# Kernel optimization log

Measured on AMD Instinct MI355X. Metric: run time of the kernel, lower is better.

Reference implementation:

```python
import jax, jax.numpy as jnp
import numpy as np


def setup_inputs() -> dict:
    key = jax.random.key(0)
    x = jax.random.normal(key, (8192, 4096), dtype=jnp.float32)
    return {"x": x, "k": 1}


def reference(x, k):
    # torch.linalg.svdvals returns singular values in descending order;
    # jnp.linalg.svd with compute_uv=False does the same.
    s = jnp.linalg.svd(x, compute_uv=False)  # [min(m, n)], descending
    return jnp.sum(s[:k] ** 2)
```

## Files before the change

kernel.cpp:

```cpp
#include <hip/hip_runtime.h>
#include <hip/hip_fp16.h>
#include <math.h>


#define NROWS 8192
#define NCOLS 4096
#define T_STEPS 16
#define NBLK 512
#define RPB 16
#define SPIN_LIMIT 200000L

typedef float f32x4_t __attribute__((ext_vector_type(4)));

__device__ __forceinline__ unsigned ic_ld_u32(const unsigned* p) {
    unsigned v;
    asm volatile("global_load_dword %0, %1, off sc0 sc1\n\ts_waitcnt vmcnt(0)"
                 : "=v"(v) : "v"(p) : "memory");
    return v;
}
__device__ __forceinline__ float ic_ld_f32(const float* p) {
    float v;
    asm volatile("global_load_dword %0, %1, off sc0 sc1\n\ts_waitcnt vmcnt(0)"
                 : "=v"(v) : "v"(p) : "memory");
    return v;
}
__device__ __forceinline__ void ic_st_u32(unsigned* p, unsigned v) {
    asm volatile("global_store_dword %0, %1, off sc0 sc1"
                 :: "v"(p), "v"(v) : "memory");
}
__device__ __forceinline__ void ic_st_f32(float* p, float v) {
    asm volatile("global_store_dword %0, %1, off sc0 sc1"
                 :: "v"(p), "v"(v) : "memory");
}
__device__ __forceinline__ void ic_st4_f32(float* p, float4 v) {
    f32x4_t x; x.x = v.x; x.y = v.y; x.z = v.z; x.w = v.w;
    asm volatile("global_store_dwordx4 %0, %1, off sc0 sc1"
                 :: "v"(p), "v"(x) : "memory");
}
__device__ __forceinline__ unsigned ic_sum4_u32(const unsigned* p0, const unsigned* p1,
                                                const unsigned* p2, const unsigned* p3) {
    unsigned a, b, c, d;
    asm volatile(
        "global_load_dword %0, %4, off sc0 sc1\n\t"
        "global_load_dword %1, %5, off sc0 sc1\n\t"
        "global_load_dword %2, %6, off sc0 sc1\n\t"
        "global_load_dword %3, %7, off sc0 sc1\n\t"
        "s_waitcnt vmcnt(0)"
        : "=&v"(a), "=&v"(b), "=&v"(c), "=&v"(d)
        : "v"(p0), "v"(p1), "v"(p2), "v"(p3) : "memory");
    return a + b + c + d;
}
__device__ __forceinline__ void ic_ld4_f32x4(const float* p0, const float* p1,
                                             const float* p2, const float* p3,
                                             float4& ao, float4& bo, float4& co, float4& do_) {
    f32x4_t a, b, c, d;
    asm volatile(
        "global_load_dwordx4 %0, %4, off sc0 sc1\n\t"
        "global_load_dwordx4 %1, %5, off sc0 sc1\n\t"
        "global_load_dwordx4 %2, %6, off sc0 sc1\n\t"
        "global_load_dwordx4 %3, %7, off sc0 sc1\n\t"
        "s_waitcnt vmcnt(0)"
        : "=&v"(a), "=&v"(b), "=&v"(c), "=&v"(d)
        : "v"(p0), "v"(p1), "v"(p2), "v"(p3) : "memory");
    ao = make_float4(a.x, a.y, a.z, a.w);
    bo = make_float4(b.x, b.y, b.z, b.w);
    co = make_float4(c.x, c.y, c.z, c.w);
    do_ = make_float4(d.x, d.y, d.z, d.w);
}

__device__ __forceinline__ void up8(const float4& p, float* f) {
    const __half2* h = (const __half2*)&p;
    float2 t0 = __half22float2(h[0]);
    float2 t1 = __half22float2(h[1]);
    float2 t2 = __half22float2(h[2]);
    float2 t3 = __half22float2(h[3]);
    f[0] = t0.x; f[1] = t0.y; f[2] = t1.x; f[3] = t1.y;
    f[4] = t2.x; f[5] = t2.y; f[6] = t3.x; f[7] = t3.y;
}
__device__ __forceinline__ float4 pack8(const float4& a, const float4& b) {
    union { float4 f4; __half2 h2[4]; } u;
    u.h2[0] = __halves2half2(__float2half_rn(a.x), __float2half_rn(a.y));
    u.h2[1] = __halves2half2(__float2half_rn(a.z), __float2half_rn(a.w));
    u.h2[2] = __halves2half2(__float2half_rn(b.x), __float2half_rn(b.y));
    u.h2[3] = __halves2half2(__float2half_rn(b.z), __float2half_rn(b.w));
    return u.f4;
}

__device__ __forceinline__ void gbar(unsigned* arrive, unsigned* release,
                                     unsigned* errw, unsigned gen, int bid) {
    __syncthreads();
    if (threadIdx.x == 0) {
        asm volatile("s_waitcnt vmcnt(0)" ::: "memory");
        __hip_atomic_fetch_add(&arrive[(bid & 7) * 16], 1u,
                               __ATOMIC_RELAXED, __HIP_MEMORY_SCOPE_AGENT);
        if (ic_ld_u32(errw) == 0) {
            long iters = 0;
            if (bid == 0) {
                const unsigned target = gen * NBLK;
                for (;;) {
                    unsigned s = ic_sum4_u32(&arrive[0], &arrive[16], &arrive[32], &arrive[48])
                               + ic_sum4_u32(&arrive[64], &arrive[80], &arrive[96], &arrive[112]);
                    if (s >= target) break;
                    if (++iters > SPIN_LIMIT) { ic_st_u32(errw, gen); break; }
                    if ((iters & 255) == 0 && ic_ld_u32(errw)) break;
                    __builtin_amdgcn_s_sleep(2);
                }
                ic_st_u32(release, gen);
            } else {
                while (ic_ld_u32(release) < gen) {
                    if (++iters > SPIN_LIMIT) { ic_st_u32(errw, gen); break; }
                    if ((iters & 255) == 0 && ic_ld_u32(errw)) break;
                    __builtin_amdgcn_s_sleep(2);
                }
            }
        }
    }
    __syncthreads();
}

__global__ __launch_bounds__(256, 2) void lanczos_fused(const float* __restrict__ A,
                                                        float* __restrict__ ws,
                                                        float* __restrict__ out) {
    __shared__ __align__(16) float smem[192];
    float* slots = ws + 12288;
    unsigned* arrive = (unsigned*)(ws + 12416);
    unsigned* release = (unsigned*)(ws + 12416) + 192;
    unsigned* errw = (unsigned*)(ws + 12416) + 200;
    float* partials = ws + 262144;
    const int tid = threadIdx.x;
    const int bid = blockIdx.x;
    const int gtid = bid * 256 + tid;
    const int cA = tid * 8, cB = 2048 + tid * 8;
    unsigned gen = 0;

    float4 arA[RPB], arB[RPB];
    {
        const float* base = A + (size_t)bid * RPB * NCOLS;
#pragma unroll
        for (int r = 0; r < RPB; ++r) {
            const float* rowp = base + (size_t)r * NCOLS;
            float4 a0 = *(const float4*)(rowp + cA);
            float4 a1 = *(const float4*)(rowp + cA + 4);
            float4 b0 = *(const float4*)(rowp + cB);
            float4 b1 = *(const float4*)(rowp + cB + 4);
            arA[r] = pack8(a0, a1);
            arB[r] = pack8(b0, b1);
        }
        if (gtid < NCOLS) {
            unsigned h = (unsigned)gtid * 2654435761u;
            h ^= h >> 16; h *= 2246822519u; h ^= h >> 13;
            ic_st_f32(ws + 4096 + gtid, (h & 1u) ? 0.015625f : -0.015625f);
            ic_st_f32(ws + gtid, 0.f);
            if (gtid < 128)
                ic_st_f32(slots + gtid, (gtid == 64 || gtid == 65) ? 1.f : 0.f);
        }
    }
    gbar(arrive, release, errw, ++gen, bid);

    for (int j = 1; j <= T_STEPS; ++j) {
        const float* rc = ws + 4096 * (j % 3);
        const float* rp = ws + 4096 * ((j + 2) % 3);
        float* wt = ws + 4096 * ((j + 1) % 3);

        {
            int lane = tid & 63;
            float inv = rsqrtf(fmaxf(ic_ld_f32(&slots[64 + j]), 1e-30f));
            float vA[8], vB[8];
            {
                float4 x, y, z, w4;
                ic_ld4_f32x4(rc + cA, rc + cA + 4, rc + cB, rc + cB + 4, x, y, z, w4);
                vA[0] = x.x * inv; vA[1] = x.y * inv; vA[2] = x.z * inv; vA[3] = x.w * inv;
                vA[4] = y.x * inv; vA[5] = y.y * inv; vA[6] = y.z * inv; vA[7] = y.w * inv;
                vB[0] = z.x * inv; vB[1] = z.y * inv; vB[2] = z.z * inv; vB[3] = z.w * inv;
                vB[4] = w4.x * inv; vB[5] = w4.y * inv; vB[6] = w4.z * inv; vB[7] = w4.w * inv;
            }
            __syncthreads();
            if (tid < RPB) smem[tid] = 0.f;
            __syncthreads();
#pragma unroll
            for (int r = 0; r < RPB; ++r) {
                float f[8];
                up8(arA[r], f);
                float sp = f[0] * vA[0] + f[1] * vA[1] + f[2] * vA[2] + f[3] * vA[3]
                         + f[4] * vA[4] + f[5] * vA[5] + f[6] * vA[6] + f[7] * vA[7];
                up8(arB[r], f);
                sp += f[0] * vB[0] + f[1] * vB[1] + f[2] * vB[2] + f[3] * vB[3]
                    + f[4] * vB[4] + f[5] * vB[5] + f[6] * vB[6] + f[7] * vB[7];
#pragma unroll
                for (int off = 32; off > 0; off >>= 1) sp += __shfl_xor(sp, off);
                if (lane == 0) atomicAdd(&smem[r], sp);
            }
            __syncthreads();
            if (tid == 0) {
                float aa = 0.f;
#pragma unroll
                for (int r = 0; r < RPB; ++r) aa += smem[r] * smem[r];
                atomicAdd(&slots[j], aa);
            }
            float wacc[16];
#pragma unroll
            for (int i = 0; i < 16; ++i) wacc[i] = 0.f;
#pragma unroll
            for (int r = 0; r < RPB; ++r) {
                float s = smem[r];
                float f[8];
                up8(arA[r], f);
                wacc[0] += s * f[0]; wacc[1] += s * f[1]; wacc[2] += s * f[2]; wacc[3] += s * f[3];
                wacc[4] += s * f[4]; wacc[5] += s * f[5]; wacc[6] += s * f[6]; wacc[7] += s * f[7];
                up8(arB[r], f);
                wacc[8] += s * f[0]; wacc[9] += s * f[1]; wacc[10] += s * f[2]; wacc[11] += s * f[3];
                wacc[12] += s * f[4]; wacc[13] += s * f[5]; wacc[14] += s * f[6]; wacc[15] += s * f[7];
            }
            float* pb = partials + (size_t)bid * NCOLS;
            ic_st4_f32(pb + cA,     make_float4(wacc[0], wacc[1], wacc[2], wacc[3]));
            ic_st4_f32(pb + cA + 4, make_float4(wacc[4], wacc[5], wacc[6], wacc[7]));
            ic_st4_f32(pb + cB,     make_float4(wacc[8], wacc[9], wacc[10], wacc[11]));
            ic_st4_f32(pb + cB + 4, make_float4(wacc[12], wacc[13], wacc[14], wacc[15]));
        }
        gbar(arrive, release, errw, ++gen, bid);

        if (j < T_STEPS) {
            {
                int q = tid & 1, p0 = tid >> 1;
                const float* pb0 = partials + (size_t)p0 * NCOLS + bid * 8 + q * 4;
                float4 v0, v1, v2, v3;
                ic_ld4_f32x4(pb0, pb0 + (size_t)128 * NCOLS,
                             pb0 + (size_t)256 * NCOLS, pb0 + (size_t)384 * NCOLS,
                             v0, v1, v2, v3);
                float4 s;
                s.x = v0.x + v1.x + v2.x + v3.x;
                s.y = v0.y + v1.y + v2.y + v3.y;
                s.z = v0.z + v1.z + v2.z + v3.z;
                s.w = v0.w + v1.w + v2.w + v3.w;
#pragma unroll
                for (int off = 2; off <= 32; off <<= 1) {
                    s.x += __shfl_xor(s.x, off);
                    s.y += __shfl_xor(s.y, off);
                    s.z += __shfl_xor(s.z, off);
                    s.w += __shfl_xor(s.w, off);
                }
                int lane = tid & 63, wv = tid >> 6;
                __syncthreads();
                if (lane < 2) *(float4*)&smem[32 + wv * 8 + lane * 4] = s;
                __syncthreads();
                if (tid < 8) {
                    int col = bid * 8 + tid;
                    float wsum = smem[32 + tid] + smem[40 + tid] + smem[48 + tid] + smem[56 + tid];
                    float a = ic_ld_f32(&slots[j]);
                    float n2j = fmaxf(ic_ld_f32(&slots[64 + j]), 1e-30f);
                    float n2m = fmaxf(ic_ld_f32(&slots[64 + j - 1]), 1e-30f);
                    float invj = rsqrtf(n2j);
                    float cb = sqrtf(n2j / n2m);
                    float rn = wsum - a * invj * ic_ld_f32(&rc[col]) - cb * ic_ld_f32(&rp[col]);
                    ic_st_f32(&wt[col], rn);
                    float p = rn * rn;
                    p += __shfl_xor(p, 1);
                    p += __shfl_xor(p, 2);
                    p += __shfl_xor(p, 4);
                    if (tid == 0) atomicAdd(&slots[64 + j + 1], p);
                }
            }
            gbar(arrive, release, errw, ++gen, bid);
        }
    }

    if (bid == 0) {
        const int t = T_STEPS;
        float* d_s = smem;
        float* e2_s = smem + 64;
        if (tid < 64) {
            d_s[tid] = (tid < t) ? ic_ld_f32(&slots[1 + tid]) : 0.f;
            e2_s[tid] = (tid < t - 1) ? ic_ld_f32(&slots[64 + tid + 2]) : 0.f;
        }
        __syncthreads();
        if (tid < 64) {
            int lane = tid;
            float e_here = sqrtf(e2_s[lane]);
            float e_prev = (lane > 0) ? sqrtf(e2_s[lane - 1]) : 0.f;
            float d = d_s[lane];
            float gersh = (lane < t) ? d + e_here + e_prev : 0.f;
            float dmax = (lane < t) ? d : 0.f;
#pragma unroll
            for (int off = 32; off > 0; off >>= 1) {
                gersh = fmaxf(gersh, __shfl_xor(gersh, off));
                dmax = fmaxf(dmax, __shfl_xor(dmax, off));
            }
            float lo = dmax, hi = gersh + 1e-3f;
            for (int round = 0; round < 3; ++round) {
                float stepw = (hi - lo) * (1.f / 64.f);
                float x = lo + stepw * (lane + 1);
                double qv = 1.0;
                int cnt = 0;
                for (int i = 0; i < t; ++i) {
                    double qi = (double)d_s[i] - (double)x - ((i > 0) ? (double)e2_s[i - 1] / qv : 0.0);
                    if (fabs(qi) < 1e-300) qi = -1e-300;
                    cnt += (qi < 0.0);
                    qv = qi;
                }
                unsigned long long m = __ballot(cnt < t);
                if (m) {
                    int h = 63 - __clzll(m);
                    lo = lo + stepw * (h + 1);
                    hi = lo + stepw;
                } else {
                    hi = lo + stepw;
                }
            }
            if (tid == 0) {
                unsigned e = ic_ld_u32(errw);
                out[0] = e ? (-1.0e7f - (float)e) : 0.5f * (lo + hi);
            }
        }
    }
}

extern "C" void kernel_launch(void* const* d_in, const int* in_sizes, int n_in,
                              void* d_out, int out_size, void* d_ws, size_t ws_size,
                              hipStream_t stream) {
    const float* A = (const float*)d_in[0];
    float* out = (float*)d_out;
    float* ws = (float*)d_ws;

    hipMemsetAsync((char*)d_ws + (size_t)12416 * 4, 0, 1024, stream);

    lanczos_fused<<<NBLK, 256, 0, stream>>>(A, ws, out);
}
```

Baseline: 911.9 us.

## Spread grid barrier counters over 64 slots with wave-parallel reduction and sharded release

Reworks the software grid barrier. Arrivals now go to 64 padded counters instead of 8. Block 0 sums them with a full wavefront load and shuffle reduction, then writes 64 sharded release flags so that waiting blocks poll different cache lines. Sleep intervals change: shorter for the master and longer for the waiters. The aim is to cut atomic contention and polling hot spots on every barrier. In exchange the master does more stores per barrier and the workspace memset grows.

```diff
diff --git a/kernel.cpp b/kernel.cpp
--- a/kernel.cpp
+++ b/kernel.cpp
@@ -36,19 +36,6 @@
     f32x4_t x; x.x = v.x; x.y = v.y; x.z = v.z; x.w = v.w;
     asm volatile("global_store_dwordx4 %0, %1, off sc0 sc1"
                  :: "v"(p), "v"(x) : "memory");
-}
-__device__ __forceinline__ unsigned ic_sum4_u32(const unsigned* p0, const unsigned* p1,
-                                                const unsigned* p2, const unsigned* p3) {
-    unsigned a, b, c, d;
-    asm volatile(
-        "global_load_dword %0, %4, off sc0 sc1\n\t"
-        "global_load_dword %1, %5, off sc0 sc1\n\t"
-        "global_load_dword %2, %6, off sc0 sc1\n\t"
-        "global_load_dword %3, %7, off sc0 sc1\n\t"
-        "s_waitcnt vmcnt(0)"
-        : "=&v"(a), "=&v"(b), "=&v"(c), "=&v"(d)
-        : "v"(p0), "v"(p1), "v"(p2), "v"(p3) : "memory");
-    return a + b + c + d;
 }
 __device__ __forceinline__ void ic_ld4_f32x4(const float* p0, const float* p1,
                                              const float* p2, const float* p3,
@@ -88,30 +75,38 @@
 
 __device__ __forceinline__ void gbar(unsigned* arrive, unsigned* release,
                                      unsigned* errw, unsigned gen, int bid) {
+    const int tid = threadIdx.x;
     __syncthreads();
-    if (threadIdx.x == 0) {
-        asm volatile("s_waitcnt vmcnt(0)" ::: "memory");
-        __hip_atomic_fetch_add(&arrive[(bid & 7) * 16], 1u,
-                               __ATOMIC_RELAXED, __HIP_MEMORY_SCOPE_AGENT);
-        if (ic_ld_u32(errw) == 0) {
+    if (tid < 64) {
+        if (tid == 0) {
+            asm volatile("s_waitcnt vmcnt(0)" ::: "memory");
+            __hip_atomic_fetch_add(&arrive[(bid & 63) * 16], 1u,
+                                   __ATOMIC_RELAXED, __HIP_MEMORY_SCOPE_AGENT);
+        }
+        if (bid == 0) {
+            const unsigned target = gen * NBLK;
             long iters = 0;
-            if (bid == 0) {
-                const unsigned target = gen * NBLK;
-                for (;;) {
-                    unsigned s = ic_sum4_u32(&arrive[0], &arrive[16], &arrive[32], &arrive[48])
-                               + ic_sum4_u32(&arrive[64], &arrive[80], &arrive[96], &arrive[112]);
-                    if (s >= target) break;
-                    if (++iters > SPIN_LIMIT) { ic_st_u32(errw, gen); break; }
-                    if ((iters & 255) == 0 && ic_ld_u32(errw)) break;
-                    __builtin_amdgcn_s_sleep(2);
-                }
-                ic_st_u32(release, gen);
-            } else {
-                while (ic_ld_u32(release) < gen) {
-                    if (++iters > SPIN_LIMIT) { ic_st_u32(errw, gen); break; }
-                    if ((iters & 255) == 0 && ic_ld_u32(errw)) break;
-                    __builtin_amdgcn_s_sleep(2);
-                }
+            for (;;) {
+                unsigned v = ic_ld_u32(&arrive[tid * 16]);
+#pragma unroll
+                for (int off = 32; off > 0; off >>= 1)
+                    v += (unsigned)__shfl_xor((int)v, off);
+                if (v >= target) break;
+                int bail = 0;
+                if (tid == 0) {
+                    if (++iters > SPIN_LIMIT) { ic_st_u32(errw, gen); bail = 1; }
+                    else if ((iters & 255) == 0 && ic_ld_u32(errw)) bail = 1;
+                }
+                if (__shfl(bail, 0)) break;
+                __builtin_amdgcn_s_sleep(1);
+            }
+            ic_st_u32(&release[tid * 16], gen);
+        } else if (tid == 0) {
+            long iters = 0;
+            while (ic_ld_u32(&release[(bid & 63) * 16]) < gen) {
+                if (++iters > SPIN_LIMIT) { ic_st_u32(errw, gen); break; }
+                if ((iters & 63) == 0 && ic_ld_u32(errw)) break;
+                __builtin_amdgcn_s_sleep(16);
             }
         }
     }
@@ -124,8 +119,8 @@
     __shared__ __align__(16) float smem[192];
     float* slots = ws + 12288;
     unsigned* arrive = (unsigned*)(ws + 12416);
-    unsigned* release = (unsigned*)(ws + 12416) + 192;
-    unsigned* errw = (unsigned*)(ws + 12416) + 200;
+    unsigned* release = (unsigned*)(ws + 12416) + 1024;
+    unsigned* errw = (unsigned*)(ws + 12416) + 2048;
     float* partials = ws + 262144;
     const int tid = threadIdx.x;
     const int bid = blockIdx.x;
@@ -321,7 +316,7 @@
     float* out = (float*)d_out;
     float* ws = (float*)d_ws;
 
-    hipMemsetAsync((char*)d_ws + (size_t)12416 * 4, 0, 1024, stream);
+    hipMemsetAsync((char*)d_ws + (size_t)12416 * 4, 0, 12288, stream);
 
     lanczos_fused<<<NBLK, 256, 0, stream>>>(A, ws, out);
 }
```

Result: slower. 945.8 us (+3.7%).
